# Performance work log

Measured on AMD Instinct MI355X. Metric: run time of the kernel, lower is better.

Reference implementation:

```python
import jax, jax.numpy as jnp
import numpy as np

N = 50000
E = 640000
R = 8


def setup_inputs() -> dict:
    key = jax.random.key(0)
    ks = jax.random.split(key, 12)
    in_c, hid_c, out_c = 128, 128, 64
    s1 = 1.0 / np.sqrt(in_c)
    s2 = 1.0 / np.sqrt(hid_c)
    s3 = 1.0 / np.sqrt(out_c)
    return {
        "x": jax.random.normal(ks[0], (N, in_c), dtype=jnp.float32),
        "edge_index": jax.random.randint(ks[1], (2, E), 0, N),
        "edge_type": jax.random.randint(ks[2], (E,), 0, R),
        # layer 1: per-relation weights, root weight, bias
        "W1": jax.random.uniform(ks[3], (R, in_c, hid_c), minval=-s1, maxval=s1, dtype=jnp.float32),
        "root1": jax.random.uniform(ks[4], (in_c, hid_c), minval=-s1, maxval=s1, dtype=jnp.float32),
        "b1": jnp.zeros((hid_c,), dtype=jnp.float32),
        # layer 2
        "W2": jax.random.uniform(ks[5], (R, hid_c, out_c), minval=-s2, maxval=s2, dtype=jnp.float32),
        "root2": jax.random.uniform(ks[6], (hid_c, out_c), minval=-s2, maxval=s2, dtype=jnp.float32),
        "b2": jnp.zeros((out_c,), dtype=jnp.float32),
        # classifier
        "Wc": jax.random.uniform(ks[7], (out_c, 2), minval=-s3, maxval=s3, dtype=jnp.float32),
        "bc": jnp.zeros((2,), dtype=jnp.float32),
    }


def _rgcn_layer(x, edge_index, edge_type, W, root, b):
    # PyG RGCNConv with aggr='mean': per relation r, mean-aggregate source
    # features over edges of type r into destinations, then apply W_r.
    # out = sum_r mean_agg_r(x) @ W_r + x @ root + b
    src, dst = edge_index[0], edge_index[1]
    msgs = x[src]  # [E, Fin] gather
    seg = edge_type * N + dst  # combined (relation, dst) segment id
    sums = jax.ops.segment_sum(msgs, seg, num_segments=R * N)  # [R*N, Fin]
    cnt = jax.ops.segment_sum(jnp.ones((msgs.shape[0],), x.dtype), seg, num_segments=R * N)
    mean = sums / jnp.maximum(cnt, 1.0)[:, None]  # zero-degree -> 0
    mean = mean.reshape(R, N, x.shape[1])  # [R, N, Fin]
    out = jnp.einsum("rnf,rfo->no", mean, W) + x @ root + b
    return out


def reference(x, edge_index, edge_type, W1, root1, b1, W2, root2, b2, Wc, bc):
    h = jax.nn.relu(_rgcn_layer(x, edge_index, edge_type, W1, root1, b1))
    # dropout (p=0.3) is identity in eval mode
    h = jax.nn.relu(_rgcn_layer(h, edge_index, edge_type, W2, root2, b2))
    logits = h @ Wc + bc  # [N, 2]
    return logits
```

## Files before the change

kernel.cpp:

```cpp
#include <hip/hip_runtime.h>

#define NN 50000
#define EE 640000
#define RR 8
#define CAP 64

typedef __bf16 bf16x8 __attribute__((ext_vector_type(8)));
typedef float  f32x4  __attribute__((ext_vector_type(4)));
typedef const __attribute__((address_space(1))) unsigned int* gas_p;
typedef __attribute__((address_space(3))) unsigned int* las_p;

__device__ __forceinline__ unsigned short f2b(float f) {
  unsigned int u = __float_as_uint(f);
  u += 0x7fffu + ((u >> 16) & 1u);
  return (unsigned short)(u >> 16);
}
__device__ __forceinline__ float b2f(unsigned short h) {
  return __uint_as_float(((unsigned int)h) << 16);
}

#define CONV_N 1600000
#define B1_N (1152 * 128)
#define B2_N (640 * 128)
__global__ void k_prologue(const float* __restrict__ x, unsigned short* __restrict__ xb,
                           const float* __restrict__ W1, const float* __restrict__ root1,
                           unsigned short* __restrict__ B1T,
                           const float* __restrict__ W2, const float* __restrict__ root2,
                           unsigned short* __restrict__ B2T,
                           int* __restrict__ cursor) {
  int t = blockIdx.x * 256 + threadIdx.x;
  if (t < CONV_N) {
    float4 v = reinterpret_cast<const float4*>(x)[t];
    ushort4 o = make_ushort4(f2b(v.x), f2b(v.y), f2b(v.z), f2b(v.w));
    reinterpret_cast<ushort4*>(xb)[t] = o;
    return;
  }
  t -= CONV_N;
  if (t < B1_N) {
    int j = t >> 7, k = t & 127;
    float v = (j < 1024) ? W1[((j >> 7) << 14) + (k << 7) + (j & 127)]
                         : root1[(k << 7) + (j - 1024)];
    B1T[t] = f2b(v);
    return;
  }
  t -= B1_N;
  if (t < B2_N) {
    int j = t >> 7, k = t & 127;
    float v = 0.0f;
    if (j < 512)      v = W2[((j >> 6) << 13) + (k << 6) + (j & 63)];
    else if (j < 576) v = root2[(k << 6) + (j - 512)];
    B2T[t] = f2b(v);
    return;
  }
  t -= B2_N;
  if (t < NN) cursor[t] = 0;
}

__global__ void k_edges(const int* __restrict__ src, const int* __restrict__ dst,
                        const int* __restrict__ typ,
                        int* __restrict__ cursor, unsigned int* __restrict__ entries) {
  int e = blockIdx.x * 256 + threadIdx.x;
  if (e >= EE) return;
  int d = dst[e], r = typ[e];
  int pos = atomicAdd(&cursor[d], 1);
  if (pos < CAP)
    entries[d * CAP + pos] = (unsigned int)src[e] | ((unsigned int)r << 16);
}

__global__ __launch_bounds__(256, 3) void k_gemm(
    const unsigned short* __restrict__ A, const unsigned short* __restrict__ BT,
    unsigned short* __restrict__ Y, float* __restrict__ rootOut,
    const float* __restrict__ bias, int M, int nsplit, int nroot, int nsub) {
  __shared__ __align__(16) unsigned short Bs[2][64 * 128];
  const int tid = threadIdx.x;
  const int m0 = blockIdx.x * 128;
  const int n0g = blockIdx.y * nsub * 64;
  const int lane = tid & 63;
  const int wave = tid >> 6;
  const int wm = (wave >> 1) << 6;
  const int wn = (wave & 1) << 5;
  const int l15 = lane & 15;
  const int quad = lane >> 4;

  {
    const unsigned short* Gb = BT + (size_t)n0g * 128;
#pragma unroll
    for (int c = 0; c < 4; ++c) {
      int L = tid + c * 256;
      int r = L >> 4, c16 = L & 15;
      int j = c16 ^ (r & 15);
      __builtin_amdgcn_global_load_lds(
          (gas_p)(const void*)(Gb + (size_t)r * 128 + j * 8),
          (las_p)(void*)(Bs[0] + r * 128 + c16 * 8), 16, 0, 0);
    }
  }

  bf16x8 af[4][4];
#pragma unroll
  for (int kk = 0; kk < 4; ++kk)
#pragma unroll
    for (int i = 0; i < 4; ++i)
      af[kk][i] = *reinterpret_cast<const bf16x8*>(
          A + (size_t)(m0 + wm + i * 16 + l15) * 128 + (kk * 4 + quad) * 8);

  __syncthreads();

  const int tr = lane >> 2;
  const int tc = lane & 3;
  const int sl0 = ((tc & 1) << 1) * 16 + tr;
  const int sl1 = sl0 + 16;
  const bool thi = (tc & 2) != 0;

  int buf = 0;
  for (int s = 0; s < nsub; ++s) {
    if (s + 1 < nsub) {
      const unsigned short* Gb = BT + (size_t)(n0g + (s + 1) * 64) * 128;
      unsigned short* Lb = Bs[buf ^ 1];
#pragma unroll
      for (int c = 0; c < 4; ++c) {
        int L = tid + c * 256;
        int r = L >> 4, c16 = L & 15;
        int j = c16 ^ (r & 15);
        __builtin_amdgcn_global_load_lds(
            (gas_p)(const void*)(Gb + (size_t)r * 128 + j * 8),
            (las_p)(void*)(Lb + r * 128 + c16 * 8), 16, 0, 0);
      }
    }

    f32x4 acc[4][2] = {};
    const unsigned short* Bc = Bs[buf];
#pragma unroll
    for (int kk = 0; kk < 4; ++kk) {
      const int sw = ((kk * 4 + quad) ^ l15) * 8;
      bf16x8 bfr[2];
#pragma unroll
      for (int j = 0; j < 2; ++j)
        bfr[j] = *reinterpret_cast<const bf16x8*>(&Bc[(wn + j * 16 + l15) * 128 + sw]);
#pragma unroll
      for (int i = 0; i < 4; ++i)
#pragma unroll
        for (int j = 0; j < 2; ++j)
          acc[i][j] = __builtin_amdgcn_mfma_f32_16x16x32_bf16(bfr[j], af[kk][i], acc[i][j], 0, 0, 0);
    }
    __syncthreads();

    const int scol = n0g + s * 64;
    if (scol >= nsplit) {
#pragma unroll
      for (int i = 0; i < 4; ++i) {
        const int m = wm + i * 16 + l15;
        if (m0 + m >= M) continue;
#pragma unroll
        for (int j = 0; j < 2; ++j) {
          const int col = scol + wn + j * 16 + quad * 4 - nsplit;
          if (col < nroot) {
            float4 b4 = *reinterpret_cast<const float4*>(&bias[col]);
            float4 v = make_float4(acc[i][j][0] + b4.x, acc[i][j][1] + b4.y,
                                   acc[i][j][2] + b4.z, acc[i][j][3] + b4.w);
            *reinterpret_cast<float4*>(&rootOut[(size_t)(m0 + m) * nroot + col]) = v;
          }
        }
      }
    } else {
#pragma unroll
      for (int i = 0; i < 4; ++i) {
        uint2 pk0, pk1;
        pk0.x = (unsigned int)f2b(acc[i][0][0]) | ((unsigned int)f2b(acc[i][0][1]) << 16);
        pk0.y = (unsigned int)f2b(acc[i][0][2]) | ((unsigned int)f2b(acc[i][0][3]) << 16);
        pk1.x = (unsigned int)f2b(acc[i][1][0]) | ((unsigned int)f2b(acc[i][1][1]) << 16);
        pk1.y = (unsigned int)f2b(acc[i][1][2]) | ((unsigned int)f2b(acc[i][1][3]) << 16);
        unsigned int a0x = __shfl(pk0.x, sl0, 64), a0y = __shfl(pk0.y, sl0, 64);
        unsigned int a1x = __shfl(pk1.x, sl0, 64), a1y = __shfl(pk1.y, sl0, 64);
        unsigned int b0x = __shfl(pk0.x, sl1, 64), b0y = __shfl(pk0.y, sl1, 64);
        unsigned int b1x = __shfl(pk1.x, sl1, 64), b1y = __shfl(pk1.y, sl1, 64);
        uint4 o;
        o.x = thi ? a1x : a0x;
        o.y = thi ? a1y : a0y;
        o.z = thi ? b1x : b0x;
        o.w = thi ? b1y : b0y;
        const int m = wm + i * 16 + tr;
        if (m0 + m < M)
          *reinterpret_cast<uint4*>(&Y[(size_t)(m0 + m) * nsplit + scol + wn + tc * 8]) = o;
      }
    }
    buf ^= 1;
  }
}

__global__ void k_agg1(const unsigned int* __restrict__ entries,
                       const int* __restrict__ cursor,
                       const unsigned short* __restrict__ y,
                       const float* __restrict__ hpre,
                       unsigned int* __restrict__ hbf) {
  const int d = blockIdx.x * 4 + (threadIdx.x >> 6);
  const int lane = threadIdx.x & 63;
  int deg = cursor[d];
  if (deg > CAP) deg = CAP;
  unsigned int e = (lane < deg) ? entries[d * CAP + lane] : 0u;
  const int myr = (e >> 16) & 7;
  float sc = 0.f;
#pragma unroll
  for (int r = 0; r < 8; ++r) {
    unsigned long long bm = __ballot(lane < deg && myr == r);
    if (myr == r) sc = __builtin_amdgcn_rcpf((float)__popcll(bm));
  }
  if (lane >= deg) sc = 0.f;

  const int g = lane >> 4;
  const int l16 = lane & 15;
  float a[8] = {};
  const int T = (deg + 7) >> 3;
  for (int t = 0; t < T; ++t) {
    const int i0 = t * 8 + g;
    const int i1 = i0 + 4;
    unsigned int e0 = __shfl(e, i0, 64);  float s0 = __shfl(sc, i0, 64);
    unsigned int e1 = __shfl(e, i1, 64);  float s1 = __shfl(sc, i1, 64);
    uint4 pk0 = *reinterpret_cast<const uint4*>(
        y + (((size_t)(e0 & 0xffffu)) << 10) + (((e0 >> 16) & 7u) << 7) + (l16 << 3));
    uint4 pk1 = *reinterpret_cast<const uint4*>(
        y + (((size_t)(e1 & 0xffffu)) << 10) + (((e1 >> 16) & 7u) << 7) + (l16 << 3));
    a[0] += b2f((unsigned short)pk0.x) * s0;
    a[1] += __uint_as_float(pk0.x & 0xffff0000u) * s0;
    a[2] += b2f((unsigned short)pk0.y) * s0;
    a[3] += __uint_as_float(pk0.y & 0xffff0000u) * s0;
    a[4] += b2f((unsigned short)pk0.z) * s0;
    a[5] += __uint_as_float(pk0.z & 0xffff0000u) * s0;
    a[6] += b2f((unsigned short)pk0.w) * s0;
    a[7] += __uint_as_float(pk0.w & 0xffff0000u) * s0;
    a[0] += b2f((unsigned short)pk1.x) * s1;
    a[1] += __uint_as_float(pk1.x & 0xffff0000u) * s1;
    a[2] += b2f((unsigned short)pk1.y) * s1;
    a[3] += __uint_as_float(pk1.y & 0xffff0000u) * s1;
    a[4] += b2f((unsigned short)pk1.z) * s1;
    a[5] += __uint_as_float(pk1.z & 0xffff0000u) * s1;
    a[6] += b2f((unsigned short)pk1.w) * s1;
    a[7] += __uint_as_float(pk1.w & 0xffff0000u) * s1;
  }
#pragma unroll
  for (int j = 0; j < 8; ++j) {
    a[j] += __shfl_xor(a[j], 16, 64);
    a[j] += __shfl_xor(a[j], 32, 64);
  }
  if (g == 0) {
    const float4* hp = reinterpret_cast<const float4*>(hpre) + (size_t)d * 32 + l16 * 2;
    float4 h0 = hp[0];
    float4 h1 = hp[1];
    float v0 = fmaxf(a[0] + h0.x, 0.f), v1 = fmaxf(a[1] + h0.y, 0.f);
    float v2 = fmaxf(a[2] + h0.z, 0.f), v3 = fmaxf(a[3] + h0.w, 0.f);
    float v4 = fmaxf(a[4] + h1.x, 0.f), v5 = fmaxf(a[5] + h1.y, 0.f);
    float v6 = fmaxf(a[6] + h1.z, 0.f), v7 = fmaxf(a[7] + h1.w, 0.f);
    uint4 o;
    o.x = (unsigned int)f2b(v0) | ((unsigned int)f2b(v1) << 16);
    o.y = (unsigned int)f2b(v2) | ((unsigned int)f2b(v3) << 16);
    o.z = (unsigned int)f2b(v4) | ((unsigned int)f2b(v5) << 16);
    o.w = (unsigned int)f2b(v6) | ((unsigned int)f2b(v7) << 16);
    reinterpret_cast<uint4*>(hbf)[(size_t)d * 16 + l16] = o;
  }
}

__global__ void k_agg2(const unsigned int* __restrict__ entries,
                       const int* __restrict__ cursor,
                       const unsigned short* __restrict__ y,
                       const float* __restrict__ hpre,
                       const float* __restrict__ Wc, const float* __restrict__ bc,
                       float* __restrict__ out) {
  const int d = blockIdx.x * 4 + (threadIdx.x >> 6);
  const int lane = threadIdx.x & 63;
  int deg = cursor[d];
  if (deg > CAP) deg = CAP;
  unsigned int e = (lane < deg) ? entries[d * CAP + lane] : 0u;
  const int myr = (e >> 16) & 7;
  float sc = 0.f;
#pragma unroll
  for (int r = 0; r < 8; ++r) {
    unsigned long long bm = __ballot(lane < deg && myr == r);
    if (myr == r) sc = __builtin_amdgcn_rcpf((float)__popcll(bm));
  }
  if (lane >= deg) sc = 0.f;

  const int g = lane >> 3;
  const int l8 = lane & 7;
  float a[8] = {};
  const int T = (deg + 15) >> 4;
  for (int t = 0; t < T; ++t) {
    const int i0 = t * 16 + g;
    const int i1 = i0 + 8;
    unsigned int e0 = __shfl(e, i0, 64);  float s0 = __shfl(sc, i0, 64);
    unsigned int e1 = __shfl(e, i1, 64);  float s1 = __shfl(sc, i1, 64);
    uint4 pk0 = *reinterpret_cast<const uint4*>(
        y + (((size_t)(e0 & 0xffffu)) << 9) + (((e0 >> 16) & 7u) << 6) + (l8 << 3));
    uint4 pk1 = *reinterpret_cast<const uint4*>(
        y + (((size_t)(e1 & 0xffffu)) << 9) + (((e1 >> 16) & 7u) << 6) + (l8 << 3));
    a[0] += b2f((unsigned short)pk0.x) * s0;
    a[1] += __uint_as_float(pk0.x & 0xffff0000u) * s0;
    a[2] += b2f((unsigned short)pk0.y) * s0;
    a[3] += __uint_as_float(pk0.y & 0xffff0000u) * s0;
    a[4] += b2f((unsigned short)pk0.z) * s0;
    a[5] += __uint_as_float(pk0.z & 0xffff0000u) * s0;
    a[6] += b2f((unsigned short)pk0.w) * s0;
    a[7] += __uint_as_float(pk0.w & 0xffff0000u) * s0;
    a[0] += b2f((unsigned short)pk1.x) * s1;
    a[1] += __uint_as_float(pk1.x & 0xffff0000u) * s1;
    a[2] += b2f((unsigned short)pk1.y) * s1;
    a[3] += __uint_as_float(pk1.y & 0xffff0000u) * s1;
    a[4] += b2f((unsigned short)pk1.z) * s1;
    a[5] += __uint_as_float(pk1.z & 0xffff0000u) * s1;
    a[6] += b2f((unsigned short)pk1.w) * s1;
    a[7] += __uint_as_float(pk1.w & 0xffff0000u) * s1;
  }
#pragma unroll
  for (int j = 0; j < 8; ++j) {
    a[j] += __shfl_xor(a[j], 8, 64);
    a[j] += __shfl_xor(a[j], 16, 64);
    a[j] += __shfl_xor(a[j], 32, 64);
  }
  const float4* hp = reinterpret_cast<const float4*>(hpre) + (size_t)d * 16 + l8 * 2;
  float4 h0 = hp[0];
  float4 h1 = hp[1];
  float v0 = fmaxf(a[0] + h0.x, 0.f), v1 = fmaxf(a[1] + h0.y, 0.f);
  float v2 = fmaxf(a[2] + h0.z, 0.f), v3 = fmaxf(a[3] + h0.w, 0.f);
  float v4 = fmaxf(a[4] + h1.x, 0.f), v5 = fmaxf(a[5] + h1.y, 0.f);
  float v6 = fmaxf(a[6] + h1.z, 0.f), v7 = fmaxf(a[7] + h1.w, 0.f);
  const float4* wc4 = reinterpret_cast<const float4*>(Wc) + l8 * 4;
  float4 w0 = wc4[0], w1 = wc4[1], w2 = wc4[2], w3 = wc4[3];
  float p0 = v0 * w0.x + v1 * w0.z + v2 * w1.x + v3 * w1.z
           + v4 * w2.x + v5 * w2.z + v6 * w3.x + v7 * w3.z;
  float p1 = v0 * w0.y + v1 * w0.w + v2 * w1.y + v3 * w1.w
           + v4 * w2.y + v5 * w2.w + v6 * w3.y + v7 * w3.w;
  p0 += __shfl_xor(p0, 1, 64); p1 += __shfl_xor(p1, 1, 64);
  p0 += __shfl_xor(p0, 2, 64); p1 += __shfl_xor(p1, 2, 64);
  p0 += __shfl_xor(p0, 4, 64); p1 += __shfl_xor(p1, 4, 64);
  if (lane == 0) {
    out[d * 2 + 0] = p0 + bc[0];
    out[d * 2 + 1] = p1 + bc[1];
  }
}

extern "C" void kernel_launch(void* const* d_in, const int* in_sizes, int n_in,
                              void* d_out, int out_size, void* d_ws, size_t ws_size,
                              hipStream_t stream) {
  const float* x     = (const float*)d_in[0];
  const int*   ei    = (const int*)d_in[1];
  const int*   et    = (const int*)d_in[2];
  const float* W1    = (const float*)d_in[3];
  const float* root1 = (const float*)d_in[4];
  const float* b1    = (const float*)d_in[5];
  const float* W2    = (const float*)d_in[6];
  const float* root2 = (const float*)d_in[7];
  const float* b2    = (const float*)d_in[8];
  const float* Wc    = (const float*)d_in[9];
  const float* bc    = (const float*)d_in[10];
  const int* srcI = ei;
  const int* dstI = ei + EE;

  char* ws = (char*)d_ws;
  unsigned short* xb      = (unsigned short*)(ws);
  unsigned int*   hbf     = (unsigned int*)(ws);
  unsigned short* B1T     = (unsigned short*)(ws + 12800000);
  unsigned short* B2T     = (unsigned short*)(ws + 13094912);
  int*            cursor  = (int*)(ws + 13258752);
  unsigned int*   entries = (unsigned int*)(ws + 13458752);
  float*          hpre    = (float*)(ws + 26258752);
  unsigned short* y1      = (unsigned short*)(ws + 51858752);
  unsigned short* y2      = y1;

  const int PRO_N = CONV_N + B1_N + B2_N + NN;
  k_prologue<<<(PRO_N + 255) / 256, 256, 0, stream>>>(x, xb, W1, root1, B1T,
                                                      W2, root2, B2T, cursor);
  k_edges<<<(EE + 255) / 256, 256, 0, stream>>>(srcI, dstI, et, cursor, entries);

  k_gemm<<<dim3(391, 3), 256, 0, stream>>>(xb, B1T, y1, hpre, b1, NN, 1024, 128, 6);
  k_agg1<<<NN / 4, 256, 0, stream>>>(entries, cursor, y1, hpre, hbf);

  k_gemm<<<dim3(391, 2), 256, 0, stream>>>((const unsigned short*)hbf, B2T, y2, hpre, b2, NN, 512, 64, 5);
  k_agg2<<<NN / 4, 256, 0, stream>>>(entries, cursor, y2, hpre, Wc, bc, (float*)d_out);
}
```

Before: 263.9 us.

## Fold edge bucketing into first GEMM launch and widen aggregation gather unroll

The separate edge-bucketing kernel is removed. Its work now runs inside the first GEMM launch on an extra grid row (blockIdx.y==0) that uses a grid-stride loop, so it overlaps with the GEMM tiles and one launch disappears. The per-relation mean scale now comes from three bit-plane ballots instead of eight per-relation ballots. Both aggregation kernels issue four gathered row loads per iteration instead of two and prefetch the root/bias rows before the loop, to raise memory-level parallelism. The risk is that the 391 edge blocks compete with the GEMM blocks for slots, and the extra loads raise register pressure.

Result: no change. 259.9 us (-1.5%).

```diff
diff --git a/kernel.cpp b/kernel.cpp
--- a/kernel.cpp
+++ b/kernel.cpp
@@ -17,6 +17,18 @@
 }
 __device__ __forceinline__ float b2f(unsigned short h) {
   return __uint_as_float(((unsigned int)h) << 16);
+}
+
+__device__ __forceinline__ float edge_scale(unsigned int e, int lane, int deg) {
+  unsigned long long valid = __ballot(lane < deg);
+  unsigned long long m0 = __ballot((e >> 16) & 1u);
+  unsigned long long m1 = __ballot((e >> 17) & 1u);
+  unsigned long long m2 = __ballot((e >> 18) & 1u);
+  unsigned long long mm = ((e >> 16) & 1u ? m0 : ~m0);
+  mm &= ((e >> 17) & 1u ? m1 : ~m1);
+  mm &= ((e >> 18) & 1u ? m2 : ~m2);
+  mm &= valid;
+  return (lane < deg) ? __builtin_amdgcn_rcpf((float)__popcll(mm)) : 0.f;
 }
 
 #define CONV_N 1600000
@@ -56,25 +68,31 @@
   if (t < NN) cursor[t] = 0;
 }
 
-__global__ void k_edges(const int* __restrict__ src, const int* __restrict__ dst,
-                        const int* __restrict__ typ,
-                        int* __restrict__ cursor, unsigned int* __restrict__ entries) {
-  int e = blockIdx.x * 256 + threadIdx.x;
-  if (e >= EE) return;
-  int d = dst[e], r = typ[e];
-  int pos = atomicAdd(&cursor[d], 1);
-  if (pos < CAP)
-    entries[d * CAP + pos] = (unsigned int)src[e] | ((unsigned int)r << 16);
-}
-
+template <bool EDGES>
 __global__ __launch_bounds__(256, 3) void k_gemm(
     const unsigned short* __restrict__ A, const unsigned short* __restrict__ BT,
     unsigned short* __restrict__ Y, float* __restrict__ rootOut,
-    const float* __restrict__ bias, int M, int nsplit, int nroot, int nsub) {
+    const float* __restrict__ bias, int M, int nsplit, int nroot, int nsub,
+    const int* __restrict__ srcI, const int* __restrict__ dstI,
+    const int* __restrict__ typ, int* __restrict__ cursor,
+    unsigned int* __restrict__ entries) {
   __shared__ __align__(16) unsigned short Bs[2][64 * 128];
   const int tid = threadIdx.x;
+
+  if (EDGES && blockIdx.y == 0) {
+    const int stride = gridDim.x * 256;
+    for (int e = blockIdx.x * 256 + tid; e < EE; e += stride) {
+      int d = dstI[e], r = typ[e];
+      int pos = atomicAdd(&cursor[d], 1);
+      if (pos < CAP)
+        entries[d * CAP + pos] = (unsigned int)srcI[e] | ((unsigned int)r << 16);
+    }
+    return;
+  }
+
   const int m0 = blockIdx.x * 128;
-  const int n0g = blockIdx.y * nsub * 64;
+  const int cg = EDGES ? (blockIdx.y - 1) : blockIdx.y;
+  const int n0g = cg * nsub * 64;
   const int lane = tid & 63;
   const int wave = tid >> 6;
   const int wm = (wave >> 1) << 6;
@@ -187,6 +205,16 @@
   }
 }
 
+#define ACC8(pk, s)                                          \
+  a[0] += b2f((unsigned short)pk.x) * s;                     \
+  a[1] += __uint_as_float(pk.x & 0xffff0000u) * s;           \
+  a[2] += b2f((unsigned short)pk.y) * s;                     \
+  a[3] += __uint_as_float(pk.y & 0xffff0000u) * s;           \
+  a[4] += b2f((unsigned short)pk.z) * s;                     \
+  a[5] += __uint_as_float(pk.z & 0xffff0000u) * s;           \
+  a[6] += b2f((unsigned short)pk.w) * s;                     \
+  a[7] += __uint_as_float(pk.w & 0xffff0000u) * s;
+
 __global__ void k_agg1(const unsigned int* __restrict__ entries,
                        const int* __restrict__ cursor,
                        const unsigned short* __restrict__ y,
@@ -197,44 +225,38 @@
   int deg = cursor[d];
   if (deg > CAP) deg = CAP;
   unsigned int e = (lane < deg) ? entries[d * CAP + lane] : 0u;
-  const int myr = (e >> 16) & 7;
-  float sc = 0.f;
-#pragma unroll
-  for (int r = 0; r < 8; ++r) {
-    unsigned long long bm = __ballot(lane < deg && myr == r);
-    if (myr == r) sc = __builtin_amdgcn_rcpf((float)__popcll(bm));
-  }
-  if (lane >= deg) sc = 0.f;
+  float sc = edge_scale(e, lane, deg);
 
   const int g = lane >> 4;
   const int l16 = lane & 15;
+
+  float4 h0, h1;
+  if (g == 0) {
+    const float4* hp = reinterpret_cast<const float4*>(hpre) + (size_t)d * 32 + l16 * 2;
+    h0 = hp[0];
+    h1 = hp[1];
+  }
+
   float a[8] = {};
-  const int T = (deg + 7) >> 3;
+  const int T = (deg + 15) >> 4;
   for (int t = 0; t < T; ++t) {
-    const int i0 = t * 8 + g;
-    const int i1 = i0 + 4;
-    unsigned int e0 = __shfl(e, i0, 64);  float s0 = __shfl(sc, i0, 64);
-    unsigned int e1 = __shfl(e, i1, 64);  float s1 = __shfl(sc, i1, 64);
-    uint4 pk0 = *reinterpret_cast<const uint4*>(
+    const int base = t * 16 + g;
+    unsigned int e0 = __shfl(e, base, 64);       float s0 = __shfl(sc, base, 64);
+    unsigned int e1 = __shfl(e, base + 4, 64);   float s1 = __shfl(sc, base + 4, 64);
+    unsigned int e2 = __shfl(e, base + 8, 64);   float s2 = __shfl(sc, base + 8, 64);
+    unsigned int e3 = __shfl(e, base + 12, 64);  float s3 = __shfl(sc, base + 12, 64);
+    uint4 p0 = *reinterpret_cast<const uint4*>(
         y + (((size_t)(e0 & 0xffffu)) << 10) + (((e0 >> 16) & 7u) << 7) + (l16 << 3));
-    uint4 pk1 = *reinterpret_cast<const uint4*>(
+    uint4 p1 = *reinterpret_cast<const uint4*>(
         y + (((size_t)(e1 & 0xffffu)) << 10) + (((e1 >> 16) & 7u) << 7) + (l16 << 3));
-    a[0] += b2f((unsigned short)pk0.x) * s0;
-    a[1] += __uint_as_float(pk0.x & 0xffff0000u) * s0;
-    a[2] += b2f((unsigned short)pk0.y) * s0;
-    a[3] += __uint_as_float(pk0.y & 0xffff0000u) * s0;
-    a[4] += b2f((unsigned short)pk0.z) * s0;
-    a[5] += __uint_as_float(pk0.z & 0xffff0000u) * s0;
-    a[6] += b2f((unsigned short)pk0.w) * s0;
-    a[7] += __uint_as_float(pk0.w & 0xffff0000u) * s0;
-    a[0] += b2f((unsigned short)pk1.x) * s1;
-    a[1] += __uint_as_float(pk1.x & 0xffff0000u) * s1;
-    a[2] += b2f((unsigned short)pk1.y) * s1;
-    a[3] += __uint_as_float(pk1.y & 0xffff0000u) * s1;
-    a[4] += b2f((unsigned short)pk1.z) * s1;
-    a[5] += __uint_as_float(pk1.z & 0xffff0000u) * s1;
-    a[6] += b2f((unsigned short)pk1.w) * s1;
-    a[7] += __uint_as_float(pk1.w & 0xffff0000u) * s1;
+    uint4 p2 = *reinterpret_cast<const uint4*>(
+        y + (((size_t)(e2 & 0xffffu)) << 10) + (((e2 >> 16) & 7u) << 7) + (l16 << 3));
+    uint4 p3 = *reinterpret_cast<const uint4*>(
+        y + (((size_t)(e3 & 0xffffu)) << 10) + (((e3 >> 16) & 7u) << 7) + (l16 << 3));
+    ACC8(p0, s0);
+    ACC8(p1, s1);
+    ACC8(p2, s2);
+    ACC8(p3, s3);
   }
 #pragma unroll
   for (int j = 0; j < 8; ++j) {
@@ -242,9 +264,6 @@
     a[j] += __shfl_xor(a[j], 32, 64);
   }
   if (g == 0) {
-    const float4* hp = reinterpret_cast<const float4*>(hpre) + (size_t)d * 32 + l16 * 2;
-    float4 h0 = hp[0];
-    float4 h1 = hp[1];
     float v0 = fmaxf(a[0] + h0.x, 0.f), v1 = fmaxf(a[1] + h0.y, 0.f);
     float v2 = fmaxf(a[2] + h0.z, 0.f), v3 = fmaxf(a[3] + h0.w, 0.f);
     float v4 = fmaxf(a[4] + h1.x, 0.f), v5 = fmaxf(a[5] + h1.y, 0.f);
@@ -269,44 +288,35 @@
   int deg = cursor[d];
   if (deg > CAP) deg = CAP;
   unsigned int e = (lane < deg) ? entries[d * CAP + lane] : 0u;
-  const int myr = (e >> 16) & 7;
-  float sc = 0.f;
-#pragma unroll
-  for (int r = 0; r < 8; ++r) {
-    unsigned long long bm = __ballot(lane < deg && myr == r);
-    if (myr == r) sc = __builtin_amdgcn_rcpf((float)__popcll(bm));
-  }
-  if (lane >= deg) sc = 0.f;
+  float sc = edge_scale(e, lane, deg);
 
   const int g = lane >> 3;
   const int l8 = lane & 7;
+
+  const float4* hp = reinterpret_cast<const float4*>(hpre) + (size_t)d * 16 + l8 * 2;
+  float4 h0 = hp[0];
+  float4 h1 = hp[1];
+
   float a[8] = {};
-  const int T = (deg + 15) >> 4;
+  const int T = (deg + 31) >> 5;
   for (int t = 0; t < T; ++t) {
-    const int i0 = t * 16 + g;
-    const int i1 = i0 + 8;
-    unsigned int e0 = __shfl(e, i0, 64);  float s0 = __shfl(sc, i0, 64);
-    unsigned int e1 = __shfl(e, i1, 64);  float s1 = __shfl(sc, i1, 64);
-    uint4 pk0 = *reinterpret_cast<const uint4*>(
+    const int base = t * 32 + g;
+    unsigned int e0 = __shfl(e, base, 64);       float s0 = __shfl(sc, base, 64);
+    unsigned int e1 = __shfl(e, base + 8, 64);   float s1 = __shfl(sc, base + 8, 64);
+    unsigned int e2 = __shfl(e, base + 16, 64);  float s2 = __shfl(sc, base + 16, 64);
+    unsigned int e3 = __shfl(e, base + 24, 64);  float s3 = __shfl(sc, base + 24, 64);
+    uint4 p0 = *reinterpret_cast<const uint4*>(
         y + (((size_t)(e0 & 0xffffu)) << 9) + (((e0 >> 16) & 7u) << 6) + (l8 << 3));
-    uint4 pk1 = *reinterpret_cast<const uint4*>(
+    uint4 p1 = *reinterpret_cast<const uint4*>(
         y + (((size_t)(e1 & 0xffffu)) << 9) + (((e1 >> 16) & 7u) << 6) + (l8 << 3));
-    a[0] += b2f((unsigned short)pk0.x) * s0;
-    a[1] += __uint_as_float(pk0.x & 0xffff0000u) * s0;
-    a[2] += b2f((unsigned short)pk0.y) * s0;
-    a[3] += __uint_as_float(pk0.y & 0xffff0000u) * s0;
-    a[4] += b2f((unsigned short)pk0.z) * s0;
-    a[5] += __uint_as_float(pk0.z & 0xffff0000u) * s0;
-    a[6] += b2f((unsigned short)pk0.w) * s0;
-    a[7] += __uint_as_float(pk0.w & 0xffff0000u) * s0;
-    a[0] += b2f((unsigned short)pk1.x) * s1;
-    a[1] += __uint_as_float(pk1.x & 0xffff0000u) * s1;
-    a[2] += b2f((unsigned short)pk1.y) * s1;
-    a[3] += __uint_as_float(pk1.y & 0xffff0000u) * s1;
-    a[4] += b2f((unsigned short)pk1.z) * s1;
-    a[5] += __uint_as_float(pk1.z & 0xffff0000u) * s1;
-    a[6] += b2f((unsigned short)pk1.w) * s1;
-    a[7] += __uint_as_float(pk1.w & 0xffff0000u) * s1;
+    uint4 p2 = *reinterpret_cast<const uint4*>(
+        y + (((size_t)(e2 & 0xffffu)) << 9) + (((e2 >> 16) & 7u) << 6) + (l8 << 3));
+    uint4 p3 = *reinterpret_cast<const uint4*>(
+        y + (((size_t)(e3 & 0xffffu)) << 9) + (((e3 >> 16) & 7u) << 6) + (l8 << 3));
+    ACC8(p0, s0);
+    ACC8(p1, s1);
+    ACC8(p2, s2);
+    ACC8(p3, s3);
   }
 #pragma unroll
   for (int j = 0; j < 8; ++j) {
@@ -314,9 +324,6 @@
     a[j] += __shfl_xor(a[j], 16, 64);
     a[j] += __shfl_xor(a[j], 32, 64);
   }
-  const float4* hp = reinterpret_cast<const float4*>(hpre) + (size_t)d * 16 + l8 * 2;
-  float4 h0 = hp[0];
-  float4 h1 = hp[1];
   float v0 = fmaxf(a[0] + h0.x, 0.f), v1 = fmaxf(a[1] + h0.y, 0.f);
   float v2 = fmaxf(a[2] + h0.z, 0.f), v3 = fmaxf(a[3] + h0.w, 0.f);
   float v4 = fmaxf(a[4] + h1.x, 0.f), v5 = fmaxf(a[5] + h1.y, 0.f);
@@ -367,11 +374,13 @@
   const int PRO_N = CONV_N + B1_N + B2_N + NN;
   k_prologue<<<(PRO_N + 255) / 256, 256, 0, stream>>>(x, xb, W1, root1, B1T,
                                                       W2, root2, B2T, cursor);
-  k_edges<<<(EE + 255) / 256, 256, 0, stream>>>(srcI, dstI, et, cursor, entries);
-
-  k_gemm<<<dim3(391, 3), 256, 0, stream>>>(xb, B1T, y1, hpre, b1, NN, 1024, 128, 6);
+
+  k_gemm<true><<<dim3(391, 4), 256, 0, stream>>>(xb, B1T, y1, hpre, b1, NN, 1024, 128, 6,
+                                                 srcI, dstI, et, cursor, entries);
   k_agg1<<<NN / 4, 256, 0, stream>>>(entries, cursor, y1, hpre, hbf);
 
-  k_gemm<<<dim3(391, 2), 256, 0, stream>>>((const unsigned short*)hbf, B2T, y2, hpre, b2, NN, 512, 64, 5);
+  k_gemm<false><<<dim3(391, 2), 256, 0, stream>>>((const unsigned short*)hbf, B2T, y2, hpre, b2,
+                                                  NN, 512, 64, 5,
+                                                  nullptr, nullptr, nullptr, nullptr, nullptr);
   k_agg2<<<NN / 4, 256, 0, stream>>>(entries, cursor, y2, hpre, Wc, bc, (float*)d_out);
 }
```
